# Kernel tuning notes

Measured on AMD Instinct MI355X. Metric: run time of the kernel, lower is better.

Reference implementation:

```python
import jax, jax.numpy as jnp
import numpy as np

ALPHA, BETA, GAMMA, DELTA, EPSILON = 1.0, 0.15, 0.05, 0.0, 0.1
C1 = (0.01 * 255.0) ** 2
C2 = (0.03 * 255.0) ** 2


def _gaussian_kernel11():
    # cv2.getGaussianKernel(11, 1.5) outer product
    g = np.exp(-((np.arange(11) - 5.0) ** 2) / (2.0 * 1.5 ** 2))
    g = g / g.sum()
    return jnp.asarray(np.outer(g, g), dtype=jnp.float32)


def _to_uint8_float(x):
    # clamp to [-1,1], map to [0,1], scale to 255, uint8 truncation (floor)
    x = jnp.clip(x, -1.0, 1.0)
    x01 = jnp.clip((x + 1.0) * 0.5, 0.0, 1.0)
    return jnp.floor(jnp.clip(x01 * 255.0, 0.0, 255.0))


def _depthwise_valid_conv(x, kern2d):
    # x: [B,C,H,W]; 11x11 gaussian, VALID padding == filter2D + [5:-5,5:-5] crop
    C = x.shape[1]
    k = jnp.broadcast_to(kern2d[None, None], (C, 1, 11, 11))
    return jax.lax.conv_general_dilated(
        x, k, window_strides=(1, 1), padding='VALID',
        dimension_numbers=('NCHW', 'OIHW', 'NCHW'), feature_group_count=C)


def _ssim_per_image(img1, img2):
    # img1/img2: [B,C,H,W] floats in [0,255]; basicsr-style SSIM per channel, mean over C
    kern = _gaussian_kernel11()
    conv = lambda t: _depthwise_valid_conv(t, kern)
    mu1, mu2 = conv(img1), conv(img2)
    mu1_sq, mu2_sq, mu1_mu2 = mu1 * mu1, mu2 * mu2, mu1 * mu2
    sigma1_sq = conv(img1 * img1) - mu1_sq
    sigma2_sq = conv(img2 * img2) - mu2_sq
    sigma12 = conv(img1 * img2) - mu1_mu2
    ssim_map = ((2.0 * mu1_mu2 + C1) * (2.0 * sigma12 + C2)) / (
        (mu1_sq + mu2_sq + C1) * (sigma1_sq + sigma2_sq + C2))
    return jnp.mean(ssim_map, axis=(1, 2, 3))  # [B]


def _psnr_per_image(img1, img2):
    mse = jnp.mean((img1 - img2) ** 2, axis=(1, 2, 3))
    psnr = 10.0 * jnp.log10((255.0 ** 2) / jnp.maximum(mse, 1e-12))
    return jnp.where(mse == 0.0, 100.0, psnr)


def setup_inputs() -> dict:
    key = jax.random.key(0)
    k1, k2 = jax.random.split(key)
    shape = (4, 1, 2048, 2048)
    pred = jax.random.normal(k1, shape, dtype=jnp.float32) * 0.5
    target = jax.random.normal(k2, shape, dtype=jnp.float32) * 0.5
    return {"pred": pred, "target": target}


def reference(pred, target):
    # L1 loss
    l1 = jnp.mean(jnp.abs(pred - target))

    # edge-aware gradient loss (finite differences along H and W)
    gx = lambda t: t[:, :, :-1, :] - t[:, :, 1:, :]
    gy = lambda t: t[:, :, :, :-1] - t[:, :, :, 1:]
    grad_loss = (jnp.mean(jnp.abs(gx(pred) - gx(target))) +
                 jnp.mean(jnp.abs(gy(pred) - gy(target))))

    # physical consistency: per-image/channel mean & unbiased std stats + range penalty
    pm = jnp.mean(pred, axis=(2, 3))
    tm = jnp.mean(target, axis=(2, 3))
    energy = jnp.mean((pm - tm) ** 2)
    n = pred.shape[2] * pred.shape[3]
    ps = jnp.sqrt(jnp.sum((pred - pm[:, :, None, None]) ** 2, axis=(2, 3)) / (n - 1))
    ts = jnp.sqrt(jnp.sum((target - tm[:, :, None, None]) ** 2, axis=(2, 3)) / (n - 1))
    dist = jnp.mean((ps - ts) ** 2)
    range_pen = jnp.mean(jax.nn.relu(jnp.abs(pred) - 1.0))
    phys = energy + 0.5 * dist + 0.1 * range_pen

    # SSIM / PSNR on uint8-quantized [0,255] images (metric path, no gradient)
    p8 = _to_uint8_float(pred)
    t8 = _to_uint8_float(target)
    ssim_mean = jnp.clip(jnp.mean(_ssim_per_image(p8, t8)), 0.0, 1.0)
    psnr_mean = jnp.mean(_psnr_per_image(p8, t8))
    ssim_loss = 1.0 - ssim_mean

    total = (ALPHA * l1 + BETA * grad_loss + GAMMA * phys +
             EPSILON * jax.lax.stop_gradient(ssim_loss))
    return total, psnr_mean, ssim_mean
```

## Files before the change

### kernel.cpp

```cpp
#include <hip/hip_runtime.h>
#include <math.h>

#define HDIM 2048
#define WDIM 2048
#define NPIX (HDIM*WDIM)
#define OUTW 2038

#define C1F 6.5025f
#define C2F 58.5225f

constexpr int TH   = 64, TW = 32;
constexpr int IN_R = 80;
constexpr int IQ_S = 72;
constexpr int IQ_H = IN_R * IQ_S;
constexpr int HT_R = 80;
constexpr int HT_A = 32 * HT_R;
constexpr int NBLK = 8192;

struct GaussW { float g[11]; };

typedef _Float16 half8 __attribute__((ext_vector_type(8)));
typedef float    f32x4 __attribute__((ext_vector_type(4)));
typedef float    f32x2 __attribute__((ext_vector_type(2)));

__device__ __forceinline__ float quant_u8f(float x) {
    float c = __builtin_amdgcn_fmed3f(x, -1.0f, 1.0f);
    return truncf((c + 1.0f) * 127.5f);
}

__device__ __forceinline__ f32x2 quant2(f32x2 x) {
    f32x2 c = { __builtin_amdgcn_fmed3f(x.x, -1.0f, 1.0f),
                __builtin_amdgcn_fmed3f(x.y, -1.0f, 1.0f) };
    f32x2 v = (c + 1.0f) * 127.5f;
    return { truncf(v.x), truncf(v.y) };
}

__device__ __forceinline__ unsigned pk2(float a, float b) {
    return __builtin_bit_cast(unsigned, __builtin_amdgcn_cvt_pkrtz(a, b));
}

__global__ __launch_bounds__(256, 6) void amsr2_fused(
        const float* __restrict__ pred, const float* __restrict__ targ,
        float* __restrict__ pr, GaussW gw)
{
    __shared__ alignas(16) _Float16 Ubuf[5 * HT_A];
    __shared__ float sred[16][10];
    _Float16* Iq = Ubuf;
    _Float16* Tg = Ubuf + 2 * IQ_H;

    const int b  = blockIdx.z;
    const int r0 = blockIdx.y * TH;
    const int c0 = blockIdx.x * TW;
    const float* pb = pred + (size_t)b * NPIX;
    const float* tb = targ + (size_t)b * NPIX;
    const bool interior = (blockIdx.y < 31) && (blockIdx.x < 63);

    if (threadIdx.x < 16) {
        int n = threadIdx.x;
#pragma unroll
        for (int i = 0; i < 16; ++i) ((unsigned*)Tg)[n * 16 + i] = 0u;
#pragma unroll
        for (int j = 0; j < 11; ++j) Tg[n * 32 + n + j] = (_Float16)gw.g[j];
    }

    float s0 = 0.f, s1 = 0.f, s2 = 0.f, s3 = 0.f, ssum = 0.f;
    f32x2 s4v = {0.f, 0.f}, s5v = {0.f, 0.f}, s6v = {0.f, 0.f},
          s7v = {0.f, 0.f}, s8v = {0.f, 0.f}, ssv = {0.f, 0.f};

    if (interior) {
#pragma unroll
        for (int i = 0; i < 2; ++i) {
            int item = threadIdx.x + i * 256;
            int r = item >> 3, d = item & 7;
            const float* prow = pb + (size_t)(r0 + r) * WDIM + (c0 + d * 4);
            const float* trow = tb + (size_t)(r0 + r) * WDIM + (c0 + d * 4);
            float4 a4 = *(const float4*)prow;
            float4 b4 = *(const float4*)trow;
            float4 ad = *(const float4*)(prow + WDIM);
            float4 bd = *(const float4*)(trow + WDIM);
            float p5 = prow[4], t5 = trow[4];

            f32x2 a01 = {a4.x, a4.y}, a23 = {a4.z, a4.w};
            f32x2 b01 = {b4.x, b4.y}, b23 = {b4.z, b4.w};
            f32x2 dd01 = a01 - b01, dd23 = a23 - b23;
            float dd4 = p5 - t5;
            f32x2 g01 = f32x2{ad.x, ad.y} - f32x2{bd.x, bd.y};
            f32x2 g23 = f32x2{ad.z, ad.w} - f32x2{bd.z, bd.w};

            s0 += fabsf(dd01.x); s0 += fabsf(dd01.y);
            s0 += fabsf(dd23.x); s0 += fabsf(dd23.y);
            s1 += fabsf(dd01.x - g01.x); s1 += fabsf(dd01.y - g01.y);
            s1 += fabsf(dd23.x - g23.x); s1 += fabsf(dd23.y - g23.y);
            s2 += fabsf(dd01.x - dd01.y); s2 += fabsf(dd01.y - dd23.x);
            s2 += fabsf(dd23.x - dd23.y); s2 += fabsf(dd23.y - dd4);
            s3 += fmaxf(fabsf(a4.x) - 1.0f, 0.0f);
            s3 += fmaxf(fabsf(a4.y) - 1.0f, 0.0f);
            s3 += fmaxf(fabsf(a4.z) - 1.0f, 0.0f);
            s3 += fmaxf(fabsf(a4.w) - 1.0f, 0.0f);
            s4v += a01; s4v += a23;
            s5v += b01; s5v += b23;
            s6v += a01 * a01; s6v += a23 * a23;
            s7v += b01 * b01; s7v += b23 * b23;
            f32x2 qp01 = quant2(a01), qp23 = quant2(a23);
            f32x2 qt01 = quant2(b01), qt23 = quant2(b23);
            f32x2 qd01 = qp01 - qt01, qd23 = qp23 - qt23;
            s8v += qd01 * qd01; s8v += qd23 * qd23;

            *(uint2*)&Iq[r * IQ_S + d * 4] =
                make_uint2(pk2(qp01.x, qp01.y), pk2(qp23.x, qp23.y));
            *(uint2*)&Iq[IQ_H + r * IQ_S + d * 4] =
                make_uint2(pk2(qt01.x, qt01.y), pk2(qt23.x, qt23.y));
        }
        {
            int h = threadIdx.x;
            int r = h >> 2, d = 8 + (h & 3);
            const float* prow = pb + (size_t)(r0 + r) * WDIM + (c0 + d * 4);
            const float* trow = tb + (size_t)(r0 + r) * WDIM + (c0 + d * 4);
            float4 a4 = *(const float4*)prow;
            float4 b4 = *(const float4*)trow;
            f32x2 qp01 = quant2(f32x2{a4.x, a4.y}), qp23 = quant2(f32x2{a4.z, a4.w});
            f32x2 qt01 = quant2(f32x2{b4.x, b4.y}), qt23 = quant2(f32x2{b4.z, b4.w});
            *(uint2*)&Iq[r * IQ_S + d * 4] =
                make_uint2(pk2(qp01.x, qp01.y), pk2(qp23.x, qp23.y));
            *(uint2*)&Iq[IQ_H + r * IQ_S + d * 4] =
                make_uint2(pk2(qt01.x, qt01.y), pk2(qt23.x, qt23.y));
        }
        if (threadIdx.x < 192) {
            int h = threadIdx.x;
            int rq = h / 12;
            int r = 64 + rq, d = h - rq * 12;
            const float* prow = pb + (size_t)(r0 + r) * WDIM + (c0 + d * 4);
            const float* trow = tb + (size_t)(r0 + r) * WDIM + (c0 + d * 4);
            float4 a4 = *(const float4*)prow;
            float4 b4 = *(const float4*)trow;
            f32x2 qp01 = quant2(f32x2{a4.x, a4.y}), qp23 = quant2(f32x2{a4.z, a4.w});
            f32x2 qt01 = quant2(f32x2{b4.x, b4.y}), qt23 = quant2(f32x2{b4.z, b4.w});
            *(uint2*)&Iq[r * IQ_S + d * 4] =
                make_uint2(pk2(qp01.x, qp01.y), pk2(qp23.x, qp23.y));
            *(uint2*)&Iq[IQ_H + r * IQ_S + d * 4] =
                make_uint2(pk2(qt01.x, qt01.y), pk2(qt23.x, qt23.y));
        }
    } else {
#pragma unroll
        for (int i = 0; i < 2; ++i) {
            int item = threadIdx.x + i * 256;
            int r = item >> 3, d = item & 7;
            int gr = r0 + r, gc = c0 + d * 4;
            const float* prow = pb + (size_t)gr * WDIM + gc;
            const float* trow = tb + (size_t)gr * WDIM + gc;
            float4 a4 = *(const float4*)prow;
            float4 b4 = *(const float4*)trow;
            bool down = gr < (HDIM - 1);
            bool hasR = (gc + 4) < WDIM;
            float4 z4 = make_float4(0.f, 0.f, 0.f, 0.f);
            float4 ad = down ? *(const float4*)(prow + WDIM) : z4;
            float4 bd = down ? *(const float4*)(trow + WDIM) : z4;
            float p5 = hasR ? prow[4] : 0.0f;
            float t5 = hasR ? trow[4] : 0.0f;
            float pv[4] = {a4.x, a4.y, a4.z, a4.w};
            float tv[4] = {b4.x, b4.y, b4.z, b4.w};
            float pd[4] = {ad.x, ad.y, ad.z, ad.w};
            float td[4] = {bd.x, bd.y, bd.z, bd.w};
            float qp[4], qt[4];
#pragma unroll
            for (int k = 0; k < 4; ++k) { qp[k] = quant_u8f(pv[k]); qt[k] = quant_u8f(tv[k]); }
#pragma unroll
            for (int k = 0; k < 4; ++k) {
                float av = pv[k], bv = tv[k];
                float dd = av - bv;
                s0 += fabsf(dd);
                s3 += fmaxf(fabsf(av) - 1.0f, 0.0f);
                s4v.x += av;  s5v.x += bv;
                s6v.x = fmaf(av, av, s6v.x);
                s7v.x = fmaf(bv, bv, s7v.x);
                if (down) s1 += fabsf(dd - (pd[k] - td[k]));
                float nr  = (k < 3) ? pv[k + 1] : p5;
                float nt2 = (k < 3) ? tv[k + 1] : t5;
                if (k < 3 || hasR) s2 += fabsf(dd - (nr - nt2));
                float qd = qp[k] - qt[k];
                s8v.x = fmaf(qd, qd, s8v.x);
            }
            *(uint2*)&Iq[r * IQ_S + d * 4] =
                make_uint2(pk2(qp[0], qp[1]), pk2(qp[2], qp[3]));
            *(uint2*)&Iq[IQ_H + r * IQ_S + d * 4] =
                make_uint2(pk2(qt[0], qt[1]), pk2(qt[2], qt[3]));
        }
#pragma unroll
        for (int ph = 0; ph < 2; ++ph) {
            int r, d;
            bool active = true;
            if (ph == 0) { int h = threadIdx.x; r = h >> 2; d = 8 + (h & 3); }
            else {
                int h = threadIdx.x;
                active = h < 192;
                int rq = h / 12;
                r = 64 + rq; d = h - rq * 12;
            }
            if (active) {
                int gr = r0 + r, gc = c0 + d * 4;
                bool rowok = gr < HDIM;
                const float* prow = pb + (size_t)gr * WDIM + gc;
                const float* trow = tb + (size_t)gr * WDIM + gc;
                float qp[4], qt[4];
                if (rowok && (gc + 3) < WDIM) {
                    float4 a4 = *(const float4*)prow;
                    float4 b4 = *(const float4*)trow;
                    qp[0]=quant_u8f(a4.x); qp[1]=quant_u8f(a4.y); qp[2]=quant_u8f(a4.z); qp[3]=quant_u8f(a4.w);
                    qt[0]=quant_u8f(b4.x); qt[1]=quant_u8f(b4.y); qt[2]=quant_u8f(b4.z); qt[3]=quant_u8f(b4.w);
                } else {
#pragma unroll
                    for (int k = 0; k < 4; ++k) {
                        bool ok = rowok && (gc + k) < WDIM;
                        qp[k] = ok ? quant_u8f(prow[k]) : 0.0f;
                        qt[k] = ok ? quant_u8f(trow[k]) : 0.0f;
                    }
                }
                *(uint2*)&Iq[r * IQ_S + d * 4] =
                    make_uint2(pk2(qp[0], qp[1]), pk2(qp[2], qp[3]));
                *(uint2*)&Iq[IQ_H + r * IQ_S + d * 4] =
                    make_uint2(pk2(qt[0], qt[1]), pk2(qt[2], qt[3]));
            }
        }
    }
    __syncthreads();

    const int lane = threadIdx.x & 63;
    const int wid  = threadIdx.x >> 6;
    const int q    = lane >> 4;
    const int ml   = lane & 15;
    const half8 gfrag = *(const half8*)&Tg[ml * 32 + q * 8];
    const f32x4 zero4 = {0.f, 0.f, 0.f, 0.f};

    const int npos = (wid < 2) ? 3 : 2;
    half8 hap[3], hat[3];
#pragma unroll
    for (int i = 0; i < 3; ++i) {
        if (i < npos) {
            int pos = wid + i * 4;
            int rb = (pos >> 1) * 16;
            int cb = pos & 1;
            int base = (rb + ml) * IQ_S + cb * 16 + q * 8;
            hap[i] = *(const half8*)&Iq[base];
            hat[i] = *(const half8*)&Iq[IQ_H + base];
        }
    }
    __syncthreads();

#pragma unroll
    for (int i = 0; i < 3; ++i) {
        if (i < npos) {
            int pos = wid + i * 4;
            int rb = (pos >> 1) * 16;
            int cb = pos & 1;
            const half8 ap = hap[i];
            const half8 at = hat[i];
            f32x4 d0 = __builtin_amdgcn_mfma_f32_16x16x32_f16(ap,      gfrag, zero4, 0, 0, 0);
            f32x4 d1 = __builtin_amdgcn_mfma_f32_16x16x32_f16(at,      gfrag, zero4, 0, 0, 0);
            f32x4 d2 = __builtin_amdgcn_mfma_f32_16x16x32_f16(ap * ap, gfrag, zero4, 0, 0, 0);
            f32x4 d3 = __builtin_amdgcn_mfma_f32_16x16x32_f16(at * at, gfrag, zero4, 0, 0, 0);
            f32x4 d4 = __builtin_amdgcn_mfma_f32_16x16x32_f16(ap * at, gfrag, zero4, 0, 0, 0);
            int hb = (cb * 16 + ml) * HT_R + rb + q * 4;
            *(uint2*)&Ubuf[0 * HT_A + hb] = make_uint2(pk2(d0[0], d0[1]), pk2(d0[2], d0[3]));
            *(uint2*)&Ubuf[1 * HT_A + hb] = make_uint2(pk2(d1[0], d1[1]), pk2(d1[2], d1[3]));
            *(uint2*)&Ubuf[2 * HT_A + hb] = make_uint2(pk2(d2[0], d2[1]), pk2(d2[2], d2[3]));
            *(uint2*)&Ubuf[3 * HT_A + hb] = make_uint2(pk2(d3[0], d3[1]), pk2(d3[2], d3[3]));
            *(uint2*)&Ubuf[4 * HT_A + hb] = make_uint2(pk2(d4[0], d4[1]), pk2(d4[2], d4[3]));
        }
    }
    __syncthreads();

    const int th_ = min(TH, OUTW - r0);
    const int tw_ = min(TW, OUTW - c0);
    for (int vp = wid; vp < 8; vp += 4) {
        int rb2 = (vp >> 1) * 16;
        int cb2 = vp & 1;
        f32x4 acc[5];
#pragma unroll
        for (int arr = 0; arr < 5; ++arr) {
            const half8 bf = *(const half8*)&Ubuf[arr * HT_A +
                                                  (cb2 * 16 + ml) * HT_R + rb2 + q * 8];
            acc[arr] = __builtin_amdgcn_mfma_f32_16x16x32_f16(gfrag, bf, zero4, 0, 0, 0);
        }
        if (interior) {
#pragma unroll
            for (int pp = 0; pp < 2; ++pp) {
                f32x2 mu1 = {acc[0][2*pp], acc[0][2*pp+1]};
                f32x2 mu2 = {acc[1][2*pp], acc[1][2*pp+1]};
                f32x2 vpp = {acc[2][2*pp], acc[2][2*pp+1]};
                f32x2 vtt = {acc[3][2*pp], acc[3][2*pp+1]};
                f32x2 vpt = {acc[4][2*pp], acc[4][2*pp+1]};
                f32x2 mu12 = mu1 * mu2, mu1s = mu1 * mu1, mu2s = mu2 * mu2;
                f32x2 sg12 = vpt - mu12, sg1 = vpp - mu1s, sg2 = vtt - mu2s;
                f32x2 num = (2.0f * mu12 + C1F) * (2.0f * sg12 + C2F);
                f32x2 den = (mu1s + mu2s + C1F) * (sg1 + sg2 + C2F);
                f32x2 rp = { __builtin_amdgcn_rcpf(den.x),
                             __builtin_amdgcn_rcpf(den.y) };
                ssv += num * rp;
            }
        } else {
            int col = cb2 * 16 + ml;
#pragma unroll
            for (int reg = 0; reg < 4; ++reg) {
                int row = rb2 + q * 4 + reg;
                if (row < th_ && col < tw_) {
                    float mu1 = acc[0][reg], mu2 = acc[1][reg];
                    float vpp = acc[2][reg], vtt = acc[3][reg], vpt = acc[4][reg];
                    float mu1s = mu1 * mu1, mu2s = mu2 * mu2, mu12 = mu1 * mu2;
                    float sg1 = vpp - mu1s, sg2 = vtt - mu2s, sg12 = vpt - mu12;
                    float num = (2.0f * mu12 + C1F) * (2.0f * sg12 + C2F);
                    float den = (mu1s + mu2s + C1F) * (sg1 + sg2 + C2F);
                    ssum += num * __builtin_amdgcn_rcpf(den);
                }
            }
        }
    }

    float st10[10];
    st10[0] = s0; st10[1] = s1; st10[2] = s2; st10[3] = s3;
    st10[4] = s4v.x + s4v.y; st10[5] = s5v.x + s5v.y;
    st10[6] = s6v.x + s6v.y; st10[7] = s7v.x + s7v.y;
    st10[8] = s8v.x + s8v.y; st10[9] = ssum + ssv.x + ssv.y;
#pragma unroll
    for (int c = 0; c < 10; ++c) {
        float v = st10[c];
        v += __shfl_xor(v, 8);
        v += __shfl_xor(v, 4);
        v += __shfl_xor(v, 2);
        v += __shfl_xor(v, 1);
        st10[c] = v;
    }
    if ((lane & 15) == 0) {
        int g = wid * 4 + (lane >> 4);
#pragma unroll
        for (int c = 0; c < 10; ++c) sred[g][c] = st10[c];
    }
    __syncthreads();
    if (threadIdx.x < 10) {
        int c = threadIdx.x;
        float t = 0.0f;
#pragma unroll
        for (int g = 0; g < 16; ++g) t += sred[g][c];
        int bid = ((b * 32) + blockIdx.y) * 64 + blockIdx.x;
        pr[c * NBLK + bid] = t;
    }
}

__global__ __launch_bounds__(256) void amsr2_final(
        const float* __restrict__ pr, float* __restrict__ out)
{
    __shared__ double seg[40];
    int wid = threadIdx.x >> 6, lane = threadIdx.x & 63;
    for (int sidx = wid; sidx < 40; sidx += 4) {
        int c = sidx >> 2, b = sidx & 3;
        const float* base = pr + c * NBLK + b * 2048;
        float4 v[8];
#pragma unroll
        for (int it = 0; it < 8; ++it)
            v[it] = *(const float4*)(base + (it * 64 + lane) * 4);
        double acc = 0.0;
#pragma unroll
        for (int it = 0; it < 8; ++it)
            acc += (double)v[it].x + (double)v[it].y + (double)v[it].z + (double)v[it].w;
        for (int off = 32; off > 0; off >>= 1) acc += __shfl_down(acc, off);
        if (lane == 0) seg[sidx] = acc;
    }
    __syncthreads();
    if (threadIdx.x != 0) return;
    const double n = (double)NPIX;
    double sum0 = 0, sum1 = 0, sum2 = 0, sum3 = 0;
    for (int b = 0; b < 4; ++b) {
        sum0 += seg[0*4+b]; sum1 += seg[1*4+b]; sum2 += seg[2*4+b]; sum3 += seg[3*4+b];
    }
    double l1   = sum0 / (4.0 * n);
    double grad = sum1 / (4.0 * 2047.0 * 2048.0) + sum2 / (4.0 * 2048.0 * 2047.0);
    double energy = 0.0, dist = 0.0, psnr_sum = 0.0, ssim_sum = 0.0;
    for (int b = 0; b < 4; ++b) {
        double Sp  = seg[4*4+b],  St  = seg[5*4+b];
        double Spp = seg[6*4+b],  Stt = seg[7*4+b];
        double Su8 = seg[8*4+b],  Sss = seg[9*4+b];
        double pm = Sp / n, tm = St / n;
        double dm = pm - tm; energy += dm * dm;
        double vp = (Spp - n * pm * pm) / (n - 1.0);
        double vt = (Stt - n * tm * tm) / (n - 1.0);
        double ps = sqrt(fmax(vp, 0.0)), ts = sqrt(fmax(vt, 0.0));
        double dd = ps - ts; dist += dd * dd;
        double mse = Su8 / n;
        double psnr = (mse == 0.0) ? 100.0 : 10.0 * log10(65025.0 / fmax(mse, 1e-12));
        psnr_sum += psnr;
        ssim_sum += Sss / ((double)OUTW * (double)OUTW);
    }
    energy *= 0.25; dist *= 0.25;
    double range_pen = sum3 / (4.0 * n);
    double phys = energy + 0.5 * dist + 0.1 * range_pen;
    double ssim_mean = fmin(fmax(ssim_sum * 0.25, 0.0), 1.0);
    double total = l1 + 0.15 * grad + 0.05 * phys + 0.1 * (1.0 - ssim_mean);
    out[0] = (float)total;
    out[1] = (float)(psnr_sum * 0.25);
    out[2] = (float)ssim_mean;
}

extern "C" void kernel_launch(void* const* d_in, const int* in_sizes, int n_in,
                              void* d_out, int out_size, void* d_ws, size_t ws_size,
                              hipStream_t stream)
{
    (void)in_sizes; (void)n_in; (void)out_size; (void)ws_size;
    const float* pred = (const float*)d_in[0];
    const float* targ = (const float*)d_in[1];
    float* out = (float*)d_out;
    float* pr  = (float*)d_ws;

    GaussW gw;
    {
        double e[11], sm = 0.0;
        for (int i = 0; i < 11; ++i) {
            double d = (double)(i - 5);
            e[i] = exp(-(d * d) / 4.5);
            sm += e[i];
        }
        for (int i = 0; i < 11; ++i) gw.g[i] = (float)(e[i] / sm);
    }

    amsr2_fused<<<dim3(64, 32, 4), 256, 0, stream>>>(pred, targ, pr, gw);
    amsr2_final<<<1, 256, 0, stream>>>(pr, out);
}
```

Before: 174.4 us.

## Merge squared-image convolutions into one channel to cut LDS and MFMA work

Result: slower. 178.1 us (+2.2%).

```diff
diff --git a/kernel.cpp b/kernel.cpp
--- a/kernel.cpp
+++ b/kernel.cpp
@@ -11,10 +11,11 @@
 
 constexpr int TH   = 64, TW = 32;
 constexpr int IN_R = 80;
-constexpr int IQ_S = 72;
+constexpr int IQ_S = 56;
 constexpr int IQ_H = IN_R * IQ_S;
 constexpr int HT_R = 80;
 constexpr int HT_A = 32 * HT_R;
+constexpr int NCH  = 4;
 constexpr int NBLK = 8192;
 
 struct GaussW { float g[11]; };
@@ -39,11 +40,11 @@
     return __builtin_bit_cast(unsigned, __builtin_amdgcn_cvt_pkrtz(a, b));
 }
 
-__global__ __launch_bounds__(256, 6) void amsr2_fused(
+__global__ __launch_bounds__(256, 7) void amsr2_fused(
         const float* __restrict__ pred, const float* __restrict__ targ,
         float* __restrict__ pr, GaussW gw)
 {
-    __shared__ alignas(16) _Float16 Ubuf[5 * HT_A];
+    __shared__ alignas(16) _Float16 Ubuf[NCH * HT_A];
     __shared__ float sred[16][10];
     _Float16* Iq = Ubuf;
     _Float16* Tg = Ubuf + 2 * IQ_H;
@@ -230,6 +231,7 @@
     const int ml   = lane & 15;
     const half8 gfrag = *(const half8*)&Tg[ml * 32 + q * 8];
     const f32x4 zero4 = {0.f, 0.f, 0.f, 0.f};
+    const _Float16 hquart = (_Float16)0.25f;
 
     const int npos = (wid < 2) ? 3 : 2;
     half8 hap[3], hat[3];
@@ -254,17 +256,17 @@
             int cb = pos & 1;
             const half8 ap = hap[i];
             const half8 at = hat[i];
+            half8 m2 = (ap * hquart) * ap;
+            m2 = (at * hquart) * at + m2;
             f32x4 d0 = __builtin_amdgcn_mfma_f32_16x16x32_f16(ap,      gfrag, zero4, 0, 0, 0);
             f32x4 d1 = __builtin_amdgcn_mfma_f32_16x16x32_f16(at,      gfrag, zero4, 0, 0, 0);
-            f32x4 d2 = __builtin_amdgcn_mfma_f32_16x16x32_f16(ap * ap, gfrag, zero4, 0, 0, 0);
-            f32x4 d3 = __builtin_amdgcn_mfma_f32_16x16x32_f16(at * at, gfrag, zero4, 0, 0, 0);
-            f32x4 d4 = __builtin_amdgcn_mfma_f32_16x16x32_f16(ap * at, gfrag, zero4, 0, 0, 0);
+            f32x4 d2 = __builtin_amdgcn_mfma_f32_16x16x32_f16(m2,      gfrag, zero4, 0, 0, 0);
+            f32x4 d3 = __builtin_amdgcn_mfma_f32_16x16x32_f16(ap * at, gfrag, zero4, 0, 0, 0);
             int hb = (cb * 16 + ml) * HT_R + rb + q * 4;
             *(uint2*)&Ubuf[0 * HT_A + hb] = make_uint2(pk2(d0[0], d0[1]), pk2(d0[2], d0[3]));
             *(uint2*)&Ubuf[1 * HT_A + hb] = make_uint2(pk2(d1[0], d1[1]), pk2(d1[2], d1[3]));
             *(uint2*)&Ubuf[2 * HT_A + hb] = make_uint2(pk2(d2[0], d2[1]), pk2(d2[2], d2[3]));
             *(uint2*)&Ubuf[3 * HT_A + hb] = make_uint2(pk2(d3[0], d3[1]), pk2(d3[2], d3[3]));
-            *(uint2*)&Ubuf[4 * HT_A + hb] = make_uint2(pk2(d4[0], d4[1]), pk2(d4[2], d4[3]));
         }
     }
     __syncthreads();
@@ -274,9 +276,9 @@
     for (int vp = wid; vp < 8; vp += 4) {
         int rb2 = (vp >> 1) * 16;
         int cb2 = vp & 1;
-        f32x4 acc[5];
-#pragma unroll
-        for (int arr = 0; arr < 5; ++arr) {
+        f32x4 acc[NCH];
+#pragma unroll
+        for (int arr = 0; arr < NCH; ++arr) {
             const half8 bf = *(const half8*)&Ubuf[arr * HT_A +
                                                   (cb2 * 16 + ml) * HT_R + rb2 + q * 8];
             acc[arr] = __builtin_amdgcn_mfma_f32_16x16x32_f16(gfrag, bf, zero4, 0, 0, 0);
@@ -286,13 +288,13 @@
             for (int pp = 0; pp < 2; ++pp) {
                 f32x2 mu1 = {acc[0][2*pp], acc[0][2*pp+1]};
                 f32x2 mu2 = {acc[1][2*pp], acc[1][2*pp+1]};
-                f32x2 vpp = {acc[2][2*pp], acc[2][2*pp+1]};
-                f32x2 vtt = {acc[3][2*pp], acc[3][2*pp+1]};
-                f32x2 vpt = {acc[4][2*pp], acc[4][2*pp+1]};
+                f32x2 h2  = {acc[2][2*pp], acc[2][2*pp+1]};
+                f32x2 h12 = {acc[3][2*pp], acc[3][2*pp+1]};
                 f32x2 mu12 = mu1 * mu2, mu1s = mu1 * mu1, mu2s = mu2 * mu2;
-                f32x2 sg12 = vpt - mu12, sg1 = vpp - mu1s, sg2 = vtt - mu2s;
+                f32x2 sg12 = h12 - mu12;
+                f32x2 sgs  = 4.0f * h2 - mu1s - mu2s;
                 f32x2 num = (2.0f * mu12 + C1F) * (2.0f * sg12 + C2F);
-                f32x2 den = (mu1s + mu2s + C1F) * (sg1 + sg2 + C2F);
+                f32x2 den = (mu1s + mu2s + C1F) * (sgs + C2F);
                 f32x2 rp = { __builtin_amdgcn_rcpf(den.x),
                              __builtin_amdgcn_rcpf(den.y) };
                 ssv += num * rp;
@@ -304,11 +306,12 @@
                 int row = rb2 + q * 4 + reg;
                 if (row < th_ && col < tw_) {
                     float mu1 = acc[0][reg], mu2 = acc[1][reg];
-                    float vpp = acc[2][reg], vtt = acc[3][reg], vpt = acc[4][reg];
+                    float h2  = acc[2][reg], h12 = acc[3][reg];
                     float mu1s = mu1 * mu1, mu2s = mu2 * mu2, mu12 = mu1 * mu2;
-                    float sg1 = vpp - mu1s, sg2 = vtt - mu2s, sg12 = vpt - mu12;
+                    float sg12 = h12 - mu12;
+                    float sgs  = 4.0f * h2 - mu1s - mu2s;
                     float num = (2.0f * mu12 + C1F) * (2.0f * sg12 + C2F);
-                    float den = (mu1s + mu2s + C1F) * (sg1 + sg2 + C2F);
+                    float den = (mu1s + mu2s + C1F) * (sgs + C2F);
                     ssum += num * __builtin_amdgcn_rcpf(den);
                 }
             }
```
